# Performance work log

Measured on AMD Instinct MI355X. Metric: run time of the kernel, lower is better.

## Reference

```python
import jax, jax.numpy as jnp
import numpy as np

N_NODES = 100000
N_EDGES = 1200000
N_GRAPHS = 500
IN_DIM, HID, OUT = 128, 64, 16


def setup_inputs() -> dict:
    key = jax.random.key(0)
    ks = jax.random.split(key, 10)
    x = jax.random.normal(ks[0], (N_NODES, IN_DIM), dtype=jnp.float32)
    edge_index = jax.random.randint(ks[1], (2, N_EDGES), 0, N_NODES, dtype=jnp.int64)
    batch = jnp.sort(jax.random.randint(ks[2], (N_NODES,), 0, N_GRAPHS, dtype=jnp.int64))
    # Glorot-style init for GCN linear weights, zero bias (PyG default)
    def glorot(k, fan_in, fan_out):
        s = jnp.sqrt(6.0 / (fan_in + fan_out))
        return jax.random.uniform(k, (fan_in, fan_out), jnp.float32, -s, s)
    W1 = glorot(ks[3], IN_DIM, HID); b1 = jnp.zeros((HID,), jnp.float32)
    W2 = glorot(ks[4], HID, HID);    b2 = jnp.zeros((HID,), jnp.float32)
    W3 = glorot(ks[5], HID, OUT);    b3 = jnp.zeros((OUT,), jnp.float32)
    return {"x": x, "edge_index": edge_index, "batch": batch,
            "W1": W1, "b1": b1, "W2": W2, "b2": b2, "W3": W3, "b3": b3}


def gcn_conv(x, src, dst, deg_inv_sqrt, W, b, n_nodes):
    # PyG GCNConv: h = x @ W; aggregate with sym-normalized A+I; add bias.
    h = x @ W  # [N, F_out]
    norm = deg_inv_sqrt[src] * deg_inv_sqrt[dst]            # [E]
    msg = h[src] * norm[:, None]                            # gather + scale
    agg = jax.ops.segment_sum(msg, dst, num_segments=n_nodes)
    agg = agg + h * (deg_inv_sqrt * deg_inv_sqrt)[:, None]  # self-loop term
    return agg + b


def reference(x, edge_index, batch, W1, b1, W2, b2, W3, b3):
    n = x.shape[0]
    src, dst = edge_index[0], edge_index[1]
    # degree of A + I (count incoming edges at dst, plus self-loop)
    deg = 1.0 + jax.ops.segment_sum(jnp.ones_like(src, dtype=x.dtype), dst, num_segments=n)
    dis = deg ** -0.5  # deg >= 1 so always finite
    h = gcn_conv(x, src, dst, dis, W1, b1, n)
    h = jax.nn.relu(h)
    h = gcn_conv(h, src, dst, dis, W2, b2, n)
    h = jax.nn.relu(h)
    h = gcn_conv(h, src, dst, dis, W3, b3, n)
    # global_mean_pool over graph ids
    sums = jax.ops.segment_sum(h, batch, num_segments=N_GRAPHS)
    counts = jax.ops.segment_sum(jnp.ones((n,), h.dtype), batch, num_segments=N_GRAPHS)
    return sums / jnp.clip(counts, 1.0)[:, None]
```

## Files before the change

### kernel.cpp

```cpp
#include <hip/hip_runtime.h>
#include <hip/hip_bf16.h>
#include <hip/hip_fp16.h>

#define IN_DIM 128
#define HID    64
#define OUTF   16
#define NGRAPH 500

#define CE    2048
#define NRNG  16
#define CAP   256
#define NG    32
#define RSZ   6272

typedef _Float16 f16x8 __attribute__((ext_vector_type(8)));
typedef float    f32x4v __attribute__((ext_vector_type(4)));

__device__ __forceinline__ uint2 f4_to_h4(float4 a) {
    __half2 lo = __floats2half2_rn(a.x, a.y);
    __half2 hi = __floats2half2_rn(a.z, a.w);
    uint2 r;
    r.x = *(unsigned*)&lo;
    r.y = *(unsigned*)&hi;
    return r;
}
__device__ __forceinline__ float4 h4_to_f4(uint2 q) {
    __half2 a = *(__half2*)&q.x, b = *(__half2*)&q.y;
    float2 fa = __half22float2(a), fb = __half22float2(b);
    return make_float4(fa.x, fa.y, fb.x, fb.y);
}
__device__ __forceinline__ void h8_to_f8(uint4 p, float4& f0, float4& f1) {
    __half2 a = *(__half2*)&p.x, b = *(__half2*)&p.y;
    __half2 c = *(__half2*)&p.z, d = *(__half2*)&p.w;
    float2 fa = __half22float2(a), fb = __half22float2(b);
    float2 fc = __half22float2(c), fd = __half22float2(d);
    f0 = make_float4(fa.x, fa.y, fb.x, fb.y);
    f1 = make_float4(fc.x, fc.y, fd.x, fd.y);
}

template<int K, int F, bool INF16>
__global__ __launch_bounds__(256, 4) void mfma_gemm_kernel(const void* __restrict__ Xv,
                                                           const float* __restrict__ W,
                                                           __half* __restrict__ Hh, int N) {
    constexpr int Kp = K + 8;
    constexpr int CT = F / 16;
    __shared__ _Float16 sA[64 * Kp];
    __shared__ _Float16 sBt[F * Kp];
    const int tid = threadIdx.x;
    const int row0 = blockIdx.x * 64;

    if (INF16) {
        const uint4* X8 = (const uint4*)Xv;
        constexpr int Q = K / 8;
        for (int i = tid; i < 64 * Q; i += 256) {
            int r = i / Q, q = i - r * Q;
            int gr = row0 + r;
            uint4 v = make_uint4(0u, 0u, 0u, 0u);
            if (gr < N) v = X8[(size_t)gr * Q + q];
            *(uint4*)&sA[r * Kp + q * 8] = v;
        }
    } else {
        const float4* X4 = (const float4*)Xv;
        constexpr int Q = K / 4;
        for (int i = tid; i < 64 * Q; i += 256) {
            int r = i / Q, q = i - r * Q;
            int gr = row0 + r;
            float4 v = {0.f, 0.f, 0.f, 0.f};
            if (gr < N) v = X4[(size_t)gr * Q + q];
            *(uint2*)&sA[r * Kp + q * 4] = f4_to_h4(v);
        }
    }
    {
        const float4* W4 = (const float4*)W;
        for (int i = tid; i < K * (F / 4); i += 256) {
            int k = i / (F / 4), c4 = i - k * (F / 4);
            float4 v = W4[i];
            sBt[(c4 * 4 + 0) * Kp + k] = (_Float16)v.x;
            sBt[(c4 * 4 + 1) * Kp + k] = (_Float16)v.y;
            sBt[(c4 * 4 + 2) * Kp + k] = (_Float16)v.z;
            sBt[(c4 * 4 + 3) * Kp + k] = (_Float16)v.w;
        }
    }
    __syncthreads();

    const int w = tid >> 6;
    const int l = tid & 63;
    const int m16 = l & 15;
    const int kg = l >> 4;

    f32x4v acc[CT];
#pragma unroll
    for (int t = 0; t < CT; ++t) acc[t] = (f32x4v){0.f, 0.f, 0.f, 0.f};

    const _Float16* pa = &sA[(w * 16 + m16) * Kp + kg * 8];
#pragma unroll
    for (int k0 = 0; k0 < K; k0 += 32) {
        f16x8 af = *(const f16x8*)(pa + k0);
#pragma unroll
        for (int t = 0; t < CT; ++t) {
            f16x8 bf = *(const f16x8*)&sBt[(t * 16 + m16) * Kp + k0 + kg * 8];
            acc[t] = __builtin_amdgcn_mfma_f32_16x16x32_f16(af, bf, acc[t], 0, 0, 0);
        }
    }
    __syncthreads();
    _Float16* sOut = sA;
#pragma unroll
    for (int t = 0; t < CT; ++t) {
#pragma unroll
        for (int r = 0; r < 4; ++r) {
            int m = w * 16 + kg * 4 + r;
            int n = t * 16 + m16;
            sOut[m * F + n] = (_Float16)acc[t][r];
        }
    }
    __syncthreads();
    constexpr int U4 = (F * 2) / 16;
    uint4* Ho = (uint4*)Hh;
    for (int i = tid; i < 64 * U4; i += 256) {
        int r = i / U4, q = i - r * U4;
        int gr = row0 + r;
        if (gr < N) Ho[(size_t)gr * U4 + q] = *(uint4*)&sOut[r * F + q * 8];
    }
}

__global__ __launch_bounds__(256) void part_kernel(const int* __restrict__ src,
                                                   const int* __restrict__ dst,
                                                   uint2* __restrict__ seg,
                                                   int* __restrict__ segcnt,
                                                   int E, int rangeSize) {
    __shared__ uint2 sSeg[NRNG][CAP];
    __shared__ int sCnt[NRNG];
    const int tid = threadIdx.x;
    if (tid < NRNG) sCnt[tid] = 0;
    __syncthreads();
    const int base = blockIdx.x * CE + tid;
    int d[8], s[8];
#pragma unroll
    for (int k = 0; k < 8; ++k) {
        int e = base + k * 256;
        d[k] = (e < E) ? dst[e] : -1;
        s[k] = (e < E) ? src[e] : 0;
    }
#pragma unroll
    for (int k = 0; k < 8; ++k) {
        if (d[k] >= 0) {
            int r = d[k] / rangeSize;
            int li = atomicAdd(&sCnt[r], 1);
            if (li < CAP) sSeg[r][li] = make_uint2((unsigned)s[k], (unsigned)d[k]);
        }
    }
    __syncthreads();
    for (int r = 0; r < NRNG; ++r) {
        int n = sCnt[r] < CAP ? sCnt[r] : CAP;
        uint2* out = seg + ((size_t)(blockIdx.x * NRNG + r)) * CAP;
        for (int i = tid; i < n; i += 256) out[i] = sSeg[r][i];
        if (tid == 0) segcnt[blockIdx.x * NRNG + r] = n;
    }
}

__global__ __launch_bounds__(256) void count_kernel(const uint2* __restrict__ seg,
                                                    const int* __restrict__ segcnt,
                                                    int* __restrict__ cnt,
                                                    int N, int rangeSize, int nchunks) {
    __shared__ int hist[RSZ];
    const int r = blockIdx.x & (NRNG - 1);
    const int g = blockIdx.x / NRNG;
    const int cpg = (nchunks + NG - 1) / NG;
    const int c0 = g * cpg;
    const int c1 = (c0 + cpg < nchunks) ? c0 + cpg : nchunks;
    for (int i = threadIdx.x; i < rangeSize; i += 256) hist[i] = 0;
    __syncthreads();
    const int base = r * rangeSize;
    for (int c = c0; c < c1; ++c) {
        const int si = c * NRNG + r;
        const int n = segcnt[si];
        const uint2* s = seg + (size_t)si * CAP;
        for (int i = threadIdx.x; i < n; i += 256)
            atomicAdd(&hist[(int)s[i].y - base], 1);
    }
    __syncthreads();
    const int lim = (base + rangeSize <= N) ? rangeSize : (N - base);
    for (int i = threadIdx.x; i < lim; i += 256)
        cnt[(size_t)g * N + base + i] = hist[i];
}

__global__ __launch_bounds__(1024) void scan1_kernel(int* __restrict__ cnt,
                                                     int* __restrict__ rowptr,
                                                     int* __restrict__ aux,
                                                     float* __restrict__ dis,
                                                     float* __restrict__ pool0, int N) {
    if (blockIdx.x == 0) {
        for (int i = threadIdx.x; i < NGRAPH * OUTF + NGRAPH; i += 1024) pool0[i] = 0.f;
    }
    __shared__ int s[1024];
    int i = blockIdx.x * 1024 + threadIdx.x;
    int v = 0;
    if (i < N) {
        int run = 0;
#pragma unroll
        for (int g = 0; g < NG; ++g) {
            const size_t idx = (size_t)g * N + i;
            int c = cnt[idx];
            cnt[idx] = run;
            run += c;
        }
        v = run;
        dis[i] = rsqrtf(1.0f + (float)v);
    }
    s[threadIdx.x] = v;
    __syncthreads();
    for (int off = 1; off < 1024; off <<= 1) {
        int t = (threadIdx.x >= off) ? s[threadIdx.x - off] : 0;
        __syncthreads();
        s[threadIdx.x] += t;
        __syncthreads();
    }
    if (i < N) rowptr[i] = s[threadIdx.x] - v;
    if (threadIdx.x == 1023) aux[blockIdx.x] = s[1023];
}

__global__ __launch_bounds__(1024) void scan3_kernel(int* __restrict__ rowptr,
                                                     const int* __restrict__ aux,
                                                     int N, int nb) {
    __shared__ int s[128];
    const int t = threadIdx.x;
    if (t < 128) s[t] = (t < nb) ? aux[t] : 0;
    __syncthreads();
    for (int off = 1; off < 128; off <<= 1) {
        int v = (t >= off && t < 128) ? s[t - off] : 0;
        __syncthreads();
        if (t < 128) s[t] += v;
        __syncthreads();
    }
    int add = (blockIdx.x == 0) ? 0 : s[blockIdx.x - 1];
    int i = blockIdx.x * 1024 + t;
    if (i < N) rowptr[i] += add;
}

__global__ __launch_bounds__(256) void scatter_kernel(const uint2* __restrict__ seg,
                                                      const int* __restrict__ segcnt,
                                                      const int* __restrict__ cntp,
                                                      const int* __restrict__ rowptr,
                                                      int* __restrict__ csr_src,
                                                      int N, int rangeSize, int nchunks) {
    __shared__ int hist[RSZ];
    const int r = blockIdx.x & (NRNG - 1);
    const int g = blockIdx.x / NRNG;
    const int cpg = (nchunks + NG - 1) / NG;
    const int c0 = g * cpg;
    const int c1 = (c0 + cpg < nchunks) ? c0 + cpg : nchunks;
    for (int i = threadIdx.x; i < rangeSize; i += 256) hist[i] = 0;
    __syncthreads();
    const int base = r * rangeSize;
    for (int c = c0; c < c1; ++c) {
        const int si = c * NRNG + r;
        const int n = segcnt[si];
        const uint2* s = seg + (size_t)si * CAP;
        for (int i = threadIdx.x; i < n; i += 256) {
            uint2 v = s[i];
            const int d = (int)v.y;
            const int rank = atomicAdd(&hist[d - base], 1);
            csr_src[rowptr[d] + cntp[(size_t)g * N + d] + rank] = (int)v.x;
        }
    }
}

__global__ __launch_bounds__(256) void agg64_kernel(const __half* __restrict__ Hh,
                                                    const int* __restrict__ rowptr,
                                                    const int* __restrict__ csr_src,
                                                    const float* __restrict__ dis,
                                                    const float4* __restrict__ b4,
                                                    uint4* __restrict__ outh, int N, int E) {
    const int tid = threadIdx.x;
    const int lane = tid & 63;
    const int node = blockIdx.x * 16 + (tid >> 6) * 4 + (lane >> 4);
    const int g2 = (lane >> 3) & 1;
    const int c = lane & 7;
    if (node >= N) return;
    const uint4* Hh4 = (const uint4*)Hh;
    float dd = dis[node];
    int i0 = rowptr[node];
    int i1 = (node + 1 < N) ? rowptr[node + 1] : E;
    float4 a0 = {0.f, 0.f, 0.f, 0.f}, a1 = {0.f, 0.f, 0.f, 0.f};
    int i = i0 + g2;
    int iB = i + 2;
    int sA = (i < i1) ? csr_src[i] : 0;
    int sB = (iB < i1) ? csr_src[iB] : 0;
    uint4 pA = make_uint4(0u, 0u, 0u, 0u);
    float wA = 0.f;
    if (i < i1) {
        pA = Hh4[(long long)sA * 8 + c];
        wA = dis[sA] * dd;
    }
    while (i < i1) {
        const int iC = i + 4;
        int sC = (iC < i1) ? csr_src[iC] : 0;
        uint4 pB = Hh4[(long long)sB * 8 + c];
        float wB = (iB < i1) ? dis[sB] * dd : 0.f;
        float4 v0, v1;
        h8_to_f8(pA, v0, v1);
        a0.x += v0.x * wA; a0.y += v0.y * wA; a0.z += v0.z * wA; a0.w += v0.w * wA;
        a1.x += v1.x * wA; a1.y += v1.y * wA; a1.z += v1.z * wA; a1.w += v1.w * wA;
        i = iB; iB = iC; sA = sB; sB = sC; pA = pB; wA = wB;
    }
    a0.x += __shfl_xor(a0.x, 8); a0.y += __shfl_xor(a0.y, 8);
    a0.z += __shfl_xor(a0.z, 8); a0.w += __shfl_xor(a0.w, 8);
    a1.x += __shfl_xor(a1.x, 8); a1.y += __shfl_xor(a1.y, 8);
    a1.z += __shfl_xor(a1.z, 8); a1.w += __shfl_xor(a1.w, 8);
    if (g2 == 0) {
        float sl = dd * dd;
        uint4 ps = Hh4[(long long)node * 8 + c];
        float4 h0, h1;
        h8_to_f8(ps, h0, h1);
        float4 bb0 = b4[2 * c], bb1 = b4[2 * c + 1];
        a0.x += h0.x * sl + bb0.x; a0.y += h0.y * sl + bb0.y;
        a0.z += h0.z * sl + bb0.z; a0.w += h0.w * sl + bb0.w;
        a1.x += h1.x * sl + bb1.x; a1.y += h1.y * sl + bb1.y;
        a1.z += h1.z * sl + bb1.z; a1.w += h1.w * sl + bb1.w;
        a0.x = fmaxf(a0.x, 0.f); a0.y = fmaxf(a0.y, 0.f);
        a0.z = fmaxf(a0.z, 0.f); a0.w = fmaxf(a0.w, 0.f);
        a1.x = fmaxf(a1.x, 0.f); a1.y = fmaxf(a1.y, 0.f);
        a1.z = fmaxf(a1.z, 0.f); a1.w = fmaxf(a1.w, 0.f);
        uint2 lo = f4_to_h4(a0), hi = f4_to_h4(a1);
        outh[(long long)node * 8 + c] = make_uint4(lo.x, lo.y, hi.x, hi.y);
    }
}

template<bool RELU>
__global__ __launch_bounds__(256) void agg16_kernel(const __half* __restrict__ Hh,
                                                    const int* __restrict__ rowptr,
                                                    const int* __restrict__ csr_src,
                                                    const float* __restrict__ dis,
                                                    const float4* __restrict__ b4,
                                                    float4* __restrict__ out4, int N, int E) {
    const int tid = threadIdx.x;
    const int lane = tid & 63;
    const int node = blockIdx.x * 32 + (tid >> 6) * 8 + (lane >> 3);
    const int g2 = (lane >> 2) & 1;
    const int c = lane & 3;
    if (node >= N) return;
    const uint2* Hh2 = (const uint2*)Hh;
    float dd = dis[node];
    int i0 = rowptr[node];
    int i1 = (node + 1 < N) ? rowptr[node + 1] : E;
    float4 acc = {0.f, 0.f, 0.f, 0.f};
    int i = i0 + g2;
    int iB = i + 2;
    int sA = (i < i1) ? csr_src[i] : 0;
    int sB = (iB < i1) ? csr_src[iB] : 0;
    uint2 pA = make_uint2(0u, 0u);
    float wA = 0.f;
    if (i < i1) {
        pA = Hh2[(long long)sA * 4 + c];
        wA = dis[sA] * dd;
    }
    while (i < i1) {
        const int iC = i + 4;
        int sC = (iC < i1) ? csr_src[iC] : 0;
        uint2 pB = Hh2[(long long)sB * 4 + c];
        float wB = (iB < i1) ? dis[sB] * dd : 0.f;
        float4 v = h4_to_f4(pA);
        acc.x += v.x * wA; acc.y += v.y * wA;
        acc.z += v.z * wA; acc.w += v.w * wA;
        i = iB; iB = iC; sA = sB; sB = sC; pA = pB; wA = wB;
    }
    acc.x += __shfl_xor(acc.x, 4);
    acc.y += __shfl_xor(acc.y, 4);
    acc.z += __shfl_xor(acc.z, 4);
    acc.w += __shfl_xor(acc.w, 4);
    if (g2 == 0) {
        float4 h = h4_to_f4(Hh2[(long long)node * 4 + c]);
        float sl = dd * dd;
        float4 bb = b4[c];
        acc.x += h.x * sl + bb.x; acc.y += h.y * sl + bb.y;
        acc.z += h.z * sl + bb.z; acc.w += h.w * sl + bb.w;
        if (RELU) {
            acc.x = fmaxf(acc.x, 0.f); acc.y = fmaxf(acc.y, 0.f);
            acc.z = fmaxf(acc.z, 0.f); acc.w = fmaxf(acc.w, 0.f);
        }
        out4[(long long)node * 4 + c] = acc;
    }
}

__global__ __launch_bounds__(256) void pool_kernel(const float4* __restrict__ H4,
                                                   const int* __restrict__ batch,
                                                   float* __restrict__ sums,
                                                   float* __restrict__ cnts, int N) {
    __shared__ float sBin[16][16];
    __shared__ float sCnt[16];
    const int t = threadIdx.x;
    sBin[t >> 4][t & 15] = 0.f;
    if (t < 16) sCnt[t] = 0.f;
    __syncthreads();
    const int n0 = blockIdx.x * 256;
    const int g0 = batch[n0];
    const int nl = t >> 2;
    const int f4 = t & 3;
    float4 acc = {0.f, 0.f, 0.f, 0.f};
    float cnt = 0.f;
    int curli = -1;
    for (int j = 0; j < 4; ++j) {
        int node = n0 + nl * 4 + j;
        if (node >= N) break;
        int li = batch[node] - g0;
        if (li != curli) {
            if (curli >= 0) {
                if (curli < 16) {
                    float* bp = &sBin[curli][f4 * 4];
                    atomicAdd(bp + 0, acc.x); atomicAdd(bp + 1, acc.y);
                    atomicAdd(bp + 2, acc.z); atomicAdd(bp + 3, acc.w);
                    if (f4 == 0) atomicAdd(&sCnt[curli], cnt);
                } else {
                    float* gp = &sums[(g0 + curli) * OUTF + f4 * 4];
                    atomicAdd(gp + 0, acc.x); atomicAdd(gp + 1, acc.y);
                    atomicAdd(gp + 2, acc.z); atomicAdd(gp + 3, acc.w);
                    if (f4 == 0) atomicAdd(&cnts[g0 + curli], cnt);
                }
            }
            acc.x = acc.y = acc.z = acc.w = 0.f; cnt = 0.f; curli = li;
        }
        float4 v = H4[(long long)node * 4 + f4];
        acc.x += v.x; acc.y += v.y; acc.z += v.z; acc.w += v.w;
        cnt += 1.f;
    }
    if (curli >= 0) {
        if (curli < 16) {
            float* bp = &sBin[curli][f4 * 4];
            atomicAdd(bp + 0, acc.x); atomicAdd(bp + 1, acc.y);
            atomicAdd(bp + 2, acc.z); atomicAdd(bp + 3, acc.w);
            if (f4 == 0) atomicAdd(&sCnt[curli], cnt);
        } else {
            float* gp = &sums[(g0 + curli) * OUTF + f4 * 4];
            atomicAdd(gp + 0, acc.x); atomicAdd(gp + 1, acc.y);
            atomicAdd(gp + 2, acc.z); atomicAdd(gp + 3, acc.w);
            if (f4 == 0) atomicAdd(&cnts[g0 + curli], cnt);
        }
    }
    __syncthreads();
    int bg = t >> 4, bf = t & 15;
    int g = g0 + bg;
    if (g < NGRAPH) {
        float v = sBin[bg][bf];
        if (v != 0.f) atomicAdd(&sums[g * OUTF + bf], v);
        if (bf == 0) {
            float c = sCnt[bg];
            if (c != 0.f) atomicAdd(&cnts[g], c);
        }
    }
}

__global__ void divide_kernel(const float* __restrict__ sums, const float* __restrict__ counts,
                              float* __restrict__ out) {
    int i = blockIdx.x * blockDim.x + threadIdx.x;
    if (i < NGRAPH * OUTF) out[i] = sums[i] / fmaxf(counts[i >> 4], 1.0f);
}

extern "C" void kernel_launch(void* const* d_in, const int* in_sizes, int n_in,
                              void* d_out, int out_size, void* d_ws, size_t ws_size,
                              hipStream_t stream) {
    const float* x     = (const float*)d_in[0];
    const int*   ei    = (const int*)d_in[1];
    const int*   batch = (const int*)d_in[2];
    const float* W1 = (const float*)d_in[3];
    const float* b1 = (const float*)d_in[4];
    const float* W2 = (const float*)d_in[5];
    const float* b2 = (const float*)d_in[6];
    const float* W3 = (const float*)d_in[7];
    const float* b3 = (const float*)d_in[8];
    float* out = (float*)d_out;

    const int N = in_sizes[2];
    const int E = in_sizes[1] / 2;
    const int* src = ei;
    const int* dst = ei + E;

    const int nchunks = (E + CE - 1) / CE;
    const int NGB = NG * NRNG;

    float*    ws      = (float*)d_ws;
    float*    dis     = ws;
    float*    bufA    = dis + N;
    float*    bufB    = bufA + (size_t)N * HID;
    float*    sums    = bufB + (size_t)N * HID;
    float*    cnts    = sums + NGRAPH * OUTF;
    int*      rowptr  = (int*)(cnts + NGRAPH);
    int*      csr_src = rowptr + N;
    int*      segcnt  = csr_src + E;
    int*      aux     = segcnt + nchunks * NRNG;
    uint2*    seg     = (uint2*)bufB;
    int*      cntmat  = (int*)bufA;
    __half*   HhA     = (__half*)bufA;
    __half*   HhB     = (__half*)bufB;

    const int B = 256;
    const int nb = (N + 1023) / 1024;
    const int rangeSize = (N + NRNG - 1) / NRNG;

    part_kernel<<<nchunks, B, 0, stream>>>(src, dst, seg, segcnt, E, rangeSize);
    count_kernel<<<NGB, B, 0, stream>>>(seg, segcnt, cntmat, N, rangeSize, nchunks);
    scan1_kernel<<<nb, 1024, 0, stream>>>(cntmat, rowptr, aux, dis, sums, N);
    scan3_kernel<<<nb, 1024, 0, stream>>>(rowptr, aux, N, nb);
    scatter_kernel<<<NGB, B, 0, stream>>>(seg, segcnt, cntmat, rowptr, csr_src, N, rangeSize, nchunks);

    const int gb = (N + 63) / 64;

    mfma_gemm_kernel<IN_DIM, HID, false><<<gb, B, 0, stream>>>(x, W1, HhA, N);
    agg64_kernel<<<(N + 15) / 16, B, 0, stream>>>(HhA, rowptr, csr_src,
                                                  dis, (const float4*)b1, (uint4*)HhB, N, E);

    mfma_gemm_kernel<HID, HID, true><<<gb, B, 0, stream>>>(HhB, W2, HhA, N);
    agg64_kernel<<<(N + 15) / 16, B, 0, stream>>>(HhA, rowptr, csr_src,
                                                  dis, (const float4*)b2, (uint4*)HhB, N, E);

    mfma_gemm_kernel<HID, OUTF, true><<<gb, B, 0, stream>>>(HhB, W3, HhA, N);
    agg16_kernel<false><<<(N + 31) / 32, B, 0, stream>>>(HhA, rowptr, csr_src,
                                                         dis, (const float4*)b3, (float4*)bufB, N, E);

    pool_kernel<<<(N + 255) / 256, B, 0, stream>>>((const float4*)bufB, batch, sums, cnts, N);
    divide_kernel<<<(NGRAPH * OUTF + B - 1) / B, B, 0, stream>>>(sums, cnts, out);
}
```

Baseline: 268.4 us.

## Fuse final aggregation with mean pooling and reuse count-pass ranks in scatter

The last-layer 16-wide aggregation now writes its per-node results into shared memory, and the graph-pooling reduction reads them there in the same kernel. This removes the intermediate N×16 float buffer round trip and one kernel launch. Separately, the count pass stores each edge's within-bucket rank in the high bits of the dst word, so the scatter pass no longer rebuilds a shared histogram with atomics. Costs: the fused kernel has 8x fewer blocks, each processing 256 nodes sequentially, which lowers parallelism for the gather. Packing the rank into 15 bits above a 17-bit node id depends on N staying below 131072 and on per-group bucket counts fitting in 15 bits.

```diff
diff --git a/kernel.cpp b/kernel.cpp
--- a/kernel.cpp
+++ b/kernel.cpp
@@ -158,7 +158,7 @@
     }
 }
 
-__global__ __launch_bounds__(256) void count_kernel(const uint2* __restrict__ seg,
+__global__ __launch_bounds__(256) void count_kernel(uint2* __restrict__ seg,
                                                     const int* __restrict__ segcnt,
                                                     int* __restrict__ cnt,
                                                     int N, int rangeSize, int nchunks) {
@@ -174,9 +174,12 @@
     for (int c = c0; c < c1; ++c) {
         const int si = c * NRNG + r;
         const int n = segcnt[si];
-        const uint2* s = seg + (size_t)si * CAP;
-        for (int i = threadIdx.x; i < n; i += 256)
-            atomicAdd(&hist[(int)s[i].y - base], 1);
+        uint2* s = seg + (size_t)si * CAP;
+        for (int i = threadIdx.x; i < n; i += 256) {
+            uint2 v = s[i];
+            int rank = atomicAdd(&hist[(int)v.y - base], 1);
+            s[i] = make_uint2(v.x, ((unsigned)rank << 17) | v.y);
+        }
     }
     __syncthreads();
     const int lim = (base + rangeSize <= N) ? rangeSize : (N - base);
@@ -243,23 +246,19 @@
                                                       const int* __restrict__ rowptr,
                                                       int* __restrict__ csr_src,
                                                       int N, int rangeSize, int nchunks) {
-    __shared__ int hist[RSZ];
     const int r = blockIdx.x & (NRNG - 1);
     const int g = blockIdx.x / NRNG;
     const int cpg = (nchunks + NG - 1) / NG;
     const int c0 = g * cpg;
     const int c1 = (c0 + cpg < nchunks) ? c0 + cpg : nchunks;
-    for (int i = threadIdx.x; i < rangeSize; i += 256) hist[i] = 0;
-    __syncthreads();
-    const int base = r * rangeSize;
     for (int c = c0; c < c1; ++c) {
         const int si = c * NRNG + r;
         const int n = segcnt[si];
         const uint2* s = seg + (size_t)si * CAP;
         for (int i = threadIdx.x; i < n; i += 256) {
             uint2 v = s[i];
-            const int d = (int)v.y;
-            const int rank = atomicAdd(&hist[d - base], 1);
+            const int d = (int)(v.y & 0x1FFFFu);
+            const int rank = (int)(v.y >> 17);
             csr_src[rowptr[d] + cntp[(size_t)g * N + d] + rank] = (int)v.x;
         }
     }
@@ -320,82 +319,77 @@
         a0.x = fmaxf(a0.x, 0.f); a0.y = fmaxf(a0.y, 0.f);
         a0.z = fmaxf(a0.z, 0.f); a0.w = fmaxf(a0.w, 0.f);
         a1.x = fmaxf(a1.x, 0.f); a1.y = fmaxf(a1.y, 0.f);
-        a1.z = fmaxf(a1.z, 0.f); a1.w = fmaxf(a1.w, 0.f);
+        a1.w = fmaxf(a1.w, 0.f); a1.z = fmaxf(a1.z, 0.f);
         uint2 lo = f4_to_h4(a0), hi = f4_to_h4(a1);
         outh[(long long)node * 8 + c] = make_uint4(lo.x, lo.y, hi.x, hi.y);
     }
 }
 
-template<bool RELU>
-__global__ __launch_bounds__(256) void agg16_kernel(const __half* __restrict__ Hh,
-                                                    const int* __restrict__ rowptr,
-                                                    const int* __restrict__ csr_src,
-                                                    const float* __restrict__ dis,
-                                                    const float4* __restrict__ b4,
-                                                    float4* __restrict__ out4, int N, int E) {
+__global__ __launch_bounds__(256) void agg_pool_kernel(const __half* __restrict__ Hin,
+                                                       const int* __restrict__ rowptr,
+                                                       const int* __restrict__ csr_src,
+                                                       const float* __restrict__ dis,
+                                                       const float4* __restrict__ b4,
+                                                       const int* __restrict__ batch,
+                                                       float* __restrict__ sums,
+                                                       float* __restrict__ cnts, int N, int E) {
+    __shared__ float sH[256 * 16];
+    __shared__ float sBin[16][16];
+    __shared__ float sCnt[16];
     const int tid = threadIdx.x;
+    const int n0 = blockIdx.x * 256;
+    sBin[tid >> 4][tid & 15] = 0.f;
+    if (tid < 16) sCnt[tid] = 0.f;
     const int lane = tid & 63;
-    const int node = blockIdx.x * 32 + (tid >> 6) * 8 + (lane >> 3);
+    const int widx = tid >> 6;
     const int g2 = (lane >> 2) & 1;
     const int c = lane & 3;
-    if (node >= N) return;
-    const uint2* Hh2 = (const uint2*)Hh;
-    float dd = dis[node];
-    int i0 = rowptr[node];
-    int i1 = (node + 1 < N) ? rowptr[node + 1] : E;
-    float4 acc = {0.f, 0.f, 0.f, 0.f};
-    int i = i0 + g2;
-    int iB = i + 2;
-    int sA = (i < i1) ? csr_src[i] : 0;
-    int sB = (iB < i1) ? csr_src[iB] : 0;
-    uint2 pA = make_uint2(0u, 0u);
-    float wA = 0.f;
-    if (i < i1) {
-        pA = Hh2[(long long)sA * 4 + c];
-        wA = dis[sA] * dd;
-    }
-    while (i < i1) {
-        const int iC = i + 4;
-        int sC = (iC < i1) ? csr_src[iC] : 0;
-        uint2 pB = Hh2[(long long)sB * 4 + c];
-        float wB = (iB < i1) ? dis[sB] * dd : 0.f;
-        float4 v = h4_to_f4(pA);
-        acc.x += v.x * wA; acc.y += v.y * wA;
-        acc.z += v.z * wA; acc.w += v.w * wA;
-        i = iB; iB = iC; sA = sB; sB = sC; pA = pB; wA = wB;
-    }
-    acc.x += __shfl_xor(acc.x, 4);
-    acc.y += __shfl_xor(acc.y, 4);
-    acc.z += __shfl_xor(acc.z, 4);
-    acc.w += __shfl_xor(acc.w, 4);
-    if (g2 == 0) {
-        float4 h = h4_to_f4(Hh2[(long long)node * 4 + c]);
-        float sl = dd * dd;
-        float4 bb = b4[c];
-        acc.x += h.x * sl + bb.x; acc.y += h.y * sl + bb.y;
-        acc.z += h.z * sl + bb.z; acc.w += h.w * sl + bb.w;
-        if (RELU) {
-            acc.x = fmaxf(acc.x, 0.f); acc.y = fmaxf(acc.y, 0.f);
-            acc.z = fmaxf(acc.z, 0.f); acc.w = fmaxf(acc.w, 0.f);
-        }
-        out4[(long long)node * 4 + c] = acc;
-    }
-}
-
-__global__ __launch_bounds__(256) void pool_kernel(const float4* __restrict__ H4,
-                                                   const int* __restrict__ batch,
-                                                   float* __restrict__ sums,
-                                                   float* __restrict__ cnts, int N) {
-    __shared__ float sBin[16][16];
-    __shared__ float sCnt[16];
-    const int t = threadIdx.x;
-    sBin[t >> 4][t & 15] = 0.f;
-    if (t < 16) sCnt[t] = 0.f;
-    __syncthreads();
-    const int n0 = blockIdx.x * 256;
+    const uint2* Hh2 = (const uint2*)Hin;
+    for (int p = 0; p < 8; ++p) {
+        const int node = n0 + p * 32 + widx * 8 + (lane >> 3);
+        if (node < N) {
+            float dd = dis[node];
+            int i0 = rowptr[node];
+            int i1 = (node + 1 < N) ? rowptr[node + 1] : E;
+            float4 acc = {0.f, 0.f, 0.f, 0.f};
+            int i = i0 + g2;
+            int iB = i + 2;
+            int sA = (i < i1) ? csr_src[i] : 0;
+            int sB = (iB < i1) ? csr_src[iB] : 0;
+            uint2 pA = make_uint2(0u, 0u);
+            float wA = 0.f;
+            if (i < i1) {
+                pA = Hh2[(long long)sA * 4 + c];
+                wA = dis[sA] * dd;
+            }
+            while (i < i1) {
+                const int iC = i + 4;
+                int sC = (iC < i1) ? csr_src[iC] : 0;
+                uint2 pB = Hh2[(long long)sB * 4 + c];
+                float wB = (iB < i1) ? dis[sB] * dd : 0.f;
+                float4 v = h4_to_f4(pA);
+                acc.x += v.x * wA; acc.y += v.y * wA;
+                acc.z += v.z * wA; acc.w += v.w * wA;
+                i = iB; iB = iC; sA = sB; sB = sC; pA = pB; wA = wB;
+            }
+            acc.x += __shfl_xor(acc.x, 4);
+            acc.y += __shfl_xor(acc.y, 4);
+            acc.z += __shfl_xor(acc.z, 4);
+            acc.w += __shfl_xor(acc.w, 4);
+            if (g2 == 0) {
+                float4 h = h4_to_f4(Hh2[(long long)node * 4 + c]);
+                float sl = dd * dd;
+                float4 bb = b4[c];
+                acc.x += h.x * sl + bb.x; acc.y += h.y * sl + bb.y;
+                acc.z += h.z * sl + bb.z; acc.w += h.w * sl + bb.w;
+                *(float4*)&sH[(node - n0) * 16 + 4 * c] = acc;
+            }
+        }
+    }
+    __syncthreads();
     const int g0 = batch[n0];
-    const int nl = t >> 2;
-    const int f4 = t & 3;
+    const int nl = tid >> 2;
+    const int f4 = tid & 3;
     float4 acc = {0.f, 0.f, 0.f, 0.f};
     float cnt = 0.f;
     int curli = -1;
@@ -419,7 +413,7 @@
             }
             acc.x = acc.y = acc.z = acc.w = 0.f; cnt = 0.f; curli = li;
         }
-        float4 v = H4[(long long)node * 4 + f4];
+        float4 v = *(const float4*)&sH[(nl * 4 + j) * 16 + f4 * 4];
         acc.x += v.x; acc.y += v.y; acc.z += v.z; acc.w += v.w;
         cnt += 1.f;
     }
@@ -437,14 +431,14 @@
         }
     }
     __syncthreads();
-    int bg = t >> 4, bf = t & 15;
+    int bg = tid >> 4, bf = tid & 15;
     int g = g0 + bg;
     if (g < NGRAPH) {
         float v = sBin[bg][bf];
         if (v != 0.f) atomicAdd(&sums[g * OUTF + bf], v);
         if (bf == 0) {
-            float c = sCnt[bg];
-            if (c != 0.f) atomicAdd(&cnts[g], c);
+            float c2 = sCnt[bg];
+            if (c2 != 0.f) atomicAdd(&cnts[g], c2);
         }
     }
 }
@@ -513,9 +507,8 @@
                                                   dis, (const float4*)b2, (uint4*)HhB, N, E);
 
     mfma_gemm_kernel<HID, OUTF, true><<<gb, B, 0, stream>>>(HhB, W3, HhA, N);
-    agg16_kernel<false><<<(N + 31) / 32, B, 0, stream>>>(HhA, rowptr, csr_src,
-                                                         dis, (const float4*)b3, (float4*)bufB, N, E);
-
-    pool_kernel<<<(N + 255) / 256, B, 0, stream>>>((const float4*)bufB, batch, sums, cnts, N);
+
+    agg_pool_kernel<<<(N + 255) / 256, B, 0, stream>>>(HhA, rowptr, csr_src, dis,
+                                                       (const float4*)b3, batch, sums, cnts, N, E);
     divide_kernel<<<(NGRAPH * OUTF + B - 1) / B, B, 0, stream>>>(sums, cnts, out);
 }
```

Result: slower. 281.5 us (+4.9%).
